# Optimization experiments

Hardware: AMD Instinct MI355X
Metric: run time of the kernel (lower is better)

Reference implementation:

```python
import jax, jax.numpy as jnp
import numpy as np

N = 50000      # nodes
E = 800000     # edges (avg degree 16)
DIN = 512      # input_dim
DH = 256       # hidden_dim
KMAX = 50      # max_clusters; K = max(5, min(50, ceil(N/50))) = 50 for N=50000


def _gcn_propagate(h, src, dst, n):
    """Symmetric-normalized GCN aggregation with self-loops (PyG GCNConv).
    h: already linearly transformed node features (n, d)."""
    loop = jnp.arange(n)
    s = jnp.concatenate([src, loop])
    d = jnp.concatenate([dst, loop])
    deg = jax.ops.segment_sum(jnp.ones_like(d, dtype=h.dtype), d, num_segments=n)
    dinv = jnp.where(deg > 0, deg ** -0.5, 0.0)
    norm = dinv[s] * dinv[d]                      # (E+N,)
    return jax.ops.segment_sum(norm[:, None] * h[s], d, num_segments=n)


def setup_inputs() -> dict:
    key = jax.random.key(0)
    ks = jax.random.split(key, 6)
    x = jax.random.normal(ks[0], (N, DIN), dtype=jnp.float32)
    edge_index = jax.random.randint(ks[1], (2, E), 0, N, dtype=jnp.int64)
    positions = jax.random.uniform(ks[2], (N, 2), dtype=jnp.float32)
    # GCNConv params (glorot-ish weights, zero bias as in PyG init)
    W1 = jax.random.normal(ks[3], (DIN, DH), dtype=jnp.float32) * np.float32(1.0 / np.sqrt(DIN))
    b1 = jnp.zeros((DH,), dtype=jnp.float32)
    W2 = jax.random.normal(ks[4], (DH, KMAX), dtype=jnp.float32) * np.float32(1.0 / np.sqrt(DH))
    b2 = jnp.zeros((KMAX,), dtype=jnp.float32)
    spatial_weight = jnp.asarray(1.0, dtype=jnp.float32)
    return {"x": x, "positions": positions, "W1": W1, "b1": b1,
            "W2": W2, "b2": b2, "spatial_weight": spatial_weight,
            "edge_index": edge_index}


def reference(x, positions, W1, b1, W2, b2, spatial_weight, edge_index):
    src, dst = edge_index[0], edge_index[1]
    n = x.shape[0]
    # layer 1: GCNConv(input_dim -> hidden_dim) + ReLU
    h = jax.nn.relu(_gcn_propagate(x @ W1, src, dst, n) + b1)
    # layer 2: GCNConv(hidden_dim -> max_clusters)
    s = _gcn_propagate(h @ W2, src, dst, n) + b2
    # K = max(5, min(50, ceil(N/50))) = 50 here -> s[:, :K] is identity slice
    S = jax.nn.softmax(s[:, :KMAX], axis=1)       # (N, K), Eq. 7
    # spatial loss (Eq. 9): softmax > 0 always, so the >0 guards are no-ops
    d2 = jnp.sum((positions[src] - positions[dst]) ** 2, axis=1)   # (E,) squared dist
    dot = jnp.sum(S[src] * S[dst], axis=1)                          # (E,) sum_k S_ik S_jk
    L_spatial = spatial_weight * jnp.sum(d2 * dot) / src.shape[0]
    return S, L_spatial
```

## Files before the change

### kernel.cpp

```cpp
#include <hip/hip_runtime.h>
#include <math.h>


typedef __attribute__((ext_vector_type(8))) short bf16x8;
typedef __attribute__((ext_vector_type(4))) float f32x4;
typedef __attribute__((ext_vector_type(4))) unsigned int u32x4;
typedef _Float16 f16;
typedef __attribute__((ext_vector_type(2))) _Float16 f16x2;
typedef __attribute__((ext_vector_type(4))) _Float16 f16x4;
typedef __attribute__((ext_vector_type(8))) _Float16 f16x8;

__device__ inline unsigned short f32_to_bf16(float f) {
    unsigned u = __float_as_uint(f);
    unsigned r = u + 0x7FFFu + ((u >> 16) & 1u);
    return (unsigned short)(r >> 16);
}
__device__ inline float bf16_to_f32(unsigned short h) {
    return __uint_as_float((unsigned)h << 16);
}

__device__ inline void glds16(const void* g, void* l) {
    __builtin_amdgcn_global_load_lds(
        (const __attribute__((address_space(1))) unsigned int*)g,
        (__attribute__((address_space(3))) unsigned int*)l, 16, 0, 0);
}

__global__ void detect_i64_kernel(const unsigned* __restrict__ w, int* __restrict__ flag) {
    __shared__ int red[256];
    int cnt = 0;
    for (int i = threadIdx.x; i < 4096; i += 256)
        cnt += (w[2 * i + 1] == 0u) ? 1 : 0;
    red[threadIdx.x] = cnt;
    __syncthreads();
    for (int s = 128; s > 0; s >>= 1) {
        if ((int)threadIdx.x < s) red[threadIdx.x] += red[threadIdx.x + s];
        __syncthreads();
    }
    if (threadIdx.x == 0) *flag = (red[0] > 2048) ? 1 : 0;
}

__global__ void convert_edges_kernel(const void* __restrict__ ei, int* __restrict__ es,
                                     int* __restrict__ ed, int* __restrict__ cnt,
                                     int E, const int* __restrict__ flag) {
    int idx = blockIdx.x * blockDim.x + threadIdx.x;
    if (idx >= 2 * E) return;
    int v;
    if (*flag) v = (int)((const long long*)ei)[idx];
    else       v = ((const int*)ei)[idx];
    if (idx < E) es[idx] = v;
    else { ed[idx - E] = v; atomicAdd(&cnt[v], 1); }
}

__global__ __launch_bounds__(1024) void scan_block_kernel(const int* __restrict__ cnt,
        int* __restrict__ row_ptr, int* __restrict__ btot, int n) {
    __shared__ int buf[1024];
    int i = blockIdx.x * 1024 + threadIdx.x;
    buf[threadIdx.x] = (i < n) ? cnt[i] : 0;
    __syncthreads();
    for (int off = 1; off < 1024; off <<= 1) {
        int t = ((int)threadIdx.x >= off) ? buf[threadIdx.x - off] : 0;
        __syncthreads();
        buf[threadIdx.x] += t;
        __syncthreads();
    }
    if (i < n) row_ptr[i + 1] = buf[threadIdx.x];
    if (threadIdx.x == 1023) btot[blockIdx.x] = buf[1023];
}

__global__ __launch_bounds__(1024) void scan_tops_kernel(int* __restrict__ btot, int nb) {
    __shared__ int buf[1024];
    buf[threadIdx.x] = ((int)threadIdx.x < nb) ? btot[threadIdx.x] : 0;
    __syncthreads();
    for (int off = 1; off < 1024; off <<= 1) {
        int t = ((int)threadIdx.x >= off) ? buf[threadIdx.x - off] : 0;
        __syncthreads();
        buf[threadIdx.x] += t;
        __syncthreads();
    }
    if ((int)threadIdx.x < nb) btot[threadIdx.x] = buf[threadIdx.x];
}

__global__ void scan_finalize_kernel(int* __restrict__ row_ptr, const int* __restrict__ btot,
        const int* __restrict__ cnt, int* __restrict__ cursor, float* __restrict__ dinv, int n) {
    int i = blockIdx.x * blockDim.x + threadIdx.x;
    if (i >= n) return;
    int blk = i >> 10;
    int off = blk ? btot[blk - 1] : 0;
    int incl = row_ptr[i + 1] + off;
    row_ptr[i + 1] = incl;
    cursor[i] = incl - cnt[i];
    dinv[i] = rsqrtf((float)(cnt[i] + 1));
    if (i == 0) row_ptr[0] = 0;
}

__global__ void scatter_kernel(const int* __restrict__ es, const int* __restrict__ ed,
                               const float* __restrict__ dinv, int* __restrict__ cursor,
                               int* __restrict__ csr_src, float* __restrict__ csr_nrm, int E) {
    int e = blockIdx.x * blockDim.x + threadIdx.x;
    if (e < E) {
        int s = es[e];
        int d = ed[e];
        int p = atomicAdd(&cursor[d], 1);
        csr_src[p] = s;
        csr_nrm[p] = dinv[s];
    }
}

__global__ void wsplit_kernel(const float* __restrict__ W,
                              unsigned short* __restrict__ Th,
                              unsigned short* __restrict__ Tl, int K, int N, int nk) {
    int idx = blockIdx.x * 256 + threadIdx.x;
    if (idx >= K * N) return;
    int k = idx / N, n = idx % N;
    float f = W[idx];
    unsigned short h = f32_to_bf16(f);
    unsigned short l = f32_to_bf16(f - bf16_to_f32(h));
    int p = n >> 7, np = n & 127, t = k >> 5, kg = (k & 31) >> 3, ke = k & 7;
    size_t o = ((size_t)((p * nk + t) * 4 + kg) << 10) + np * 8 + ke;
    Th[o] = h;
    Tl[o] = l;
}

__global__ void wsplit2_kernel(const float* __restrict__ W2,
                               f16* __restrict__ W2t_hi, f16* __restrict__ W2t_lo,
                               int K, int NC) {
    int idx = blockIdx.x * 256 + threadIdx.x;
    if (idx >= 64 * K) return;
    int n = idx / K, k = idx % K;
    float v = (n < NC) ? W2[(size_t)k * NC + n] : 0.f;
    f16 h = (f16)v;
    W2t_hi[idx] = h;
    W2t_lo[idx] = (f16)(v - (float)h);
}

#define G1_BM 128
#define G1_BN 128
#define G1_BK 32

__global__ __launch_bounds__(256) void gemm1_mfma(
        const float* __restrict__ X, const unsigned short* __restrict__ WtH,
        const unsigned short* __restrict__ WtL, f16* __restrict__ C,
        int M, int K, int N) {
    __shared__ __align__(16) unsigned char lds[32768];

    const int tid  = threadIdx.x;
    const int lane = tid & 63;
    const int wave = tid >> 6;
    const int wm   = wave & 1;
    const int wn   = wave >> 1;
    const int m0   = blockIdx.x * G1_BM;
    const int pn   = blockIdx.y;
    const int nk   = K / G1_BK;

    const float* Xbase[4];
    #pragma unroll
    for (int i = 0; i < 4; ++i) {
        int c   = i * 256 + tid;
        int row = c >> 3;
        int sl  = (c & 7) ^ (row & 7);
        int gr  = m0 + row;
        if (gr > M - 1) gr = M - 1;
        Xbase[i] = X + (size_t)gr * K + sl * 4;
    }
    const unsigned short* BhBase = WtH + ((size_t)pn * nk << 12) + (size_t)tid * 8;
    const unsigned short* BlBase = WtL + ((size_t)pn * nk << 12) + (size_t)tid * 8;

    f32x4 acc[4][4] = {};
    const int kq   = lane >> 4;
    const int frow = lane & 15;
    const int bOff = 16384 + (kq << 11) + ((wn * 64 + frow) << 4);

    for (int t = 0; t < nk; ++t) {
        const int k0 = t * G1_BK;
        #pragma unroll
        for (int i = 0; i < 4; ++i)
            glds16(Xbase[i] + k0, lds + i * 4096 + wave * 1024);
        const unsigned short* bh = BhBase + (size_t)t * 4096;
        const unsigned short* bl = BlBase + (size_t)t * 4096;
        glds16(bh,        lds + 16384 + wave * 1024);
        glds16(bh + 2048, lds + 20480 + wave * 1024);
        glds16(bl,        lds + 24576 + wave * 1024);
        glds16(bl + 2048, lds + 28672 + wave * 1024);
        __syncthreads();

        bf16x8 bhf[4], blf[4];
        #pragma unroll
        for (int nn = 0; nn < 4; ++nn) {
            bhf[nn] = *(const bf16x8*)(lds + bOff + nn * 256);
            blf[nn] = *(const bf16x8*)(lds + bOff + 8192 + nn * 256);
        }
        #pragma unroll
        for (int mm = 0; mm < 4; ++mm) {
            int ra = wm * 64 + mm * 16 + frow;
            int rb = ra << 7;
            int sw = (ra & 7) << 4;
            int s0 = kq << 1;
            f32x4 p0 = *(const f32x4*)(lds + rb + ((s0 << 4) ^ sw));
            f32x4 p1 = *(const f32x4*)(lds + rb + (((s0 + 1) << 4) ^ sw));
            float f[8] = {p0[0], p0[1], p0[2], p0[3], p1[0], p1[1], p1[2], p1[3]};
            u32x4 hv, lv;
            #pragma unroll
            for (int p = 0; p < 4; ++p) {
                unsigned b0 = __float_as_uint(f[2 * p]);
                unsigned b1 = __float_as_uint(f[2 * p + 1]);
                hv[p] = __builtin_amdgcn_perm(b1, b0, 0x07060302u);
                float l0 = f[2 * p]     - __uint_as_float(b0 & 0xFFFF0000u);
                float l1 = f[2 * p + 1] - __uint_as_float(b1 & 0xFFFF0000u);
                lv[p] = __builtin_amdgcn_perm(__float_as_uint(l1),
                                              __float_as_uint(l0), 0x07060302u);
            }
            union { u32x4 u; bf16x8 b; } ah, al;
            ah.u = hv; al.u = lv;
            #pragma unroll
            for (int nn = 0; nn < 4; ++nn)
                acc[mm][nn] = __builtin_amdgcn_mfma_f32_16x16x32_bf16(ah.b, bhf[nn], acc[mm][nn], 0, 0, 0);
            #pragma unroll
            for (int nn = 0; nn < 4; ++nn)
                acc[mm][nn] = __builtin_amdgcn_mfma_f32_16x16x32_bf16(ah.b, blf[nn], acc[mm][nn], 0, 0, 0);
            #pragma unroll
            for (int nn = 0; nn < 4; ++nn)
                acc[mm][nn] = __builtin_amdgcn_mfma_f32_16x16x32_bf16(al.b, bhf[nn], acc[mm][nn], 0, 0, 0);
        }
        __syncthreads();
    }

    const int n0 = pn * G1_BN;
    #pragma unroll
    for (int mm = 0; mm < 4; ++mm) {
        #pragma unroll
        for (int i = 0; i < 4; ++i) {
            int gr = m0 + wm * 64 + mm * 16 + kq * 4 + i;
            if (gr >= M) continue;
            #pragma unroll
            for (int nn = 0; nn < 4; ++nn) {
                int gc = n0 + wn * 64 + nn * 16 + frow;
                C[(size_t)gr * N + gc] = (f16)acc[mm][nn][i];
            }
        }
    }
}

__device__ inline float4 ld_h4(const f16x4* __restrict__ p) {
    f16x4 v = *p;
    return make_float4((float)v.x, (float)v.y, (float)v.z, (float)v.w);
}

__global__ __launch_bounds__(256) void agg1_gemm2_kernel(
        const f16* __restrict__ h0, const float* __restrict__ dinv,
        const int* __restrict__ row_ptr, const int* __restrict__ csr_src,
        const float* __restrict__ csr_nrm, const float* __restrict__ b1,
        const f16* __restrict__ W2t_hi, const f16* __restrict__ W2t_lo,
        f16* __restrict__ g, int n, int K, int KC) {
    __shared__ __align__(16) f16 hs[32][264];

    const int tid  = threadIdx.x;
    const int lane = tid & 63;
    const int wave = tid >> 6;
    const int base = blockIdx.x * 32;

    const f16x4* h0v = (const f16x4*)h0;
    float4 bb = ((const float4*)b1)[lane];
    for (int i = 0; i < 8; ++i) {
        int wid = base + wave * 8 + i;
        f16x4 out = {0, 0, 0, 0};
        if (wid < n) {
            float di = dinv[wid];
            float4 v = ld_h4(&h0v[(size_t)wid * 64 + lane]);
            float self = di * di;
            float4 acc;
            acc.x = self * v.x; acc.y = self * v.y; acc.z = self * v.z; acc.w = self * v.w;
            int beg = row_ptr[wid], end = row_ptr[wid + 1];
            int j = beg;
            for (; j + 4 <= end; j += 4) {
                int s0 = csr_src[j],     s1 = csr_src[j + 1];
                int s2 = csr_src[j + 2], s3 = csr_src[j + 3];
                float n0 = csr_nrm[j] * di,     n1 = csr_nrm[j + 1] * di;
                float n2 = csr_nrm[j + 2] * di, n3 = csr_nrm[j + 3] * di;
                float4 u0 = ld_h4(&h0v[(size_t)s0 * 64 + lane]);
                float4 u1 = ld_h4(&h0v[(size_t)s1 * 64 + lane]);
                float4 u2 = ld_h4(&h0v[(size_t)s2 * 64 + lane]);
                float4 u3 = ld_h4(&h0v[(size_t)s3 * 64 + lane]);
                acc.x = fmaf(n0, u0.x, acc.x); acc.y = fmaf(n0, u0.y, acc.y);
                acc.z = fmaf(n0, u0.z, acc.z); acc.w = fmaf(n0, u0.w, acc.w);
                acc.x = fmaf(n1, u1.x, acc.x); acc.y = fmaf(n1, u1.y, acc.y);
                acc.z = fmaf(n1, u1.z, acc.z); acc.w = fmaf(n1, u1.w, acc.w);
                acc.x = fmaf(n2, u2.x, acc.x); acc.y = fmaf(n2, u2.y, acc.y);
                acc.z = fmaf(n2, u2.z, acc.z); acc.w = fmaf(n2, u2.w, acc.w);
                acc.x = fmaf(n3, u3.x, acc.x); acc.y = fmaf(n3, u3.y, acc.y);
                acc.z = fmaf(n3, u3.z, acc.z); acc.w = fmaf(n3, u3.w, acc.w);
            }
            for (; j < end; ++j) {
                int s0 = csr_src[j];
                float n0 = csr_nrm[j] * di;
                float4 u0 = ld_h4(&h0v[(size_t)s0 * 64 + lane]);
                acc.x = fmaf(n0, u0.x, acc.x); acc.y = fmaf(n0, u0.y, acc.y);
                acc.z = fmaf(n0, u0.z, acc.z); acc.w = fmaf(n0, u0.w, acc.w);
            }
            out.x = (f16)fmaxf(acc.x + bb.x, 0.f);
            out.y = (f16)fmaxf(acc.y + bb.y, 0.f);
            out.z = (f16)fmaxf(acc.z + bb.z, 0.f);
            out.w = (f16)fmaxf(acc.w + bb.w, 0.f);
        }
        *(f16x4*)&hs[wave * 8 + i][lane * 4] = out;
    }
    __syncthreads();

    const int wm   = wave & 1;
    const int wn   = wave >> 1;
    const int kq   = lane >> 4;
    const int frow = lane & 15;
    const int koff = kq * 8;

    f32x4 acc2[2] = {};
    const f16* bh_base[2];
    const f16* bl_base[2];
    #pragma unroll
    for (int nn = 0; nn < 2; ++nn) {
        int r = wn * 32 + nn * 16 + frow;
        bh_base[nn] = W2t_hi + (size_t)r * K + koff;
        bl_base[nn] = W2t_lo + (size_t)r * K + koff;
    }

    for (int t = 0; t < K / 32; ++t) {
        const int kk = t * 32;
        f16x8 a = *(const f16x8*)&hs[wm * 16 + frow][kk + koff];
        #pragma unroll
        for (int nn = 0; nn < 2; ++nn) {
            f16x8 bh = *(const f16x8*)(bh_base[nn] + kk);
            f16x8 bl = *(const f16x8*)(bl_base[nn] + kk);
            acc2[nn] = __builtin_amdgcn_mfma_f32_16x16x32_f16(a, bh, acc2[nn], 0, 0, 0);
            acc2[nn] = __builtin_amdgcn_mfma_f32_16x16x32_f16(a, bl, acc2[nn], 0, 0, 0);
        }
    }

    #pragma unroll
    for (int i = 0; i < 4; ++i) {
        int gr = base + wm * 16 + kq * 4 + i;
        if (gr >= n) continue;
        #pragma unroll
        for (int nn = 0; nn < 2; ++nn) {
            int gc = wn * 32 + nn * 16 + frow;
            if (gc < KC) g[(size_t)gr * KC + gc] = (f16)acc2[nn][i];
        }
    }
}

__global__ __launch_bounds__(256) void agg2_softmax_kernel(const f16* __restrict__ g,
        const float* __restrict__ dinv, const int* __restrict__ row_ptr,
        const int* __restrict__ csr_src, const float* __restrict__ csr_nrm,
        const float* __restrict__ b2, float* __restrict__ S, f16* __restrict__ Sh,
        int n, int KC) {
    int wid = (int)((blockIdx.x * (size_t)blockDim.x + threadIdx.x) >> 6);
    int lane = threadIdx.x & 63;
    if (wid >= n) return;
    bool act = lane < KC;
    size_t gidx = act ? (size_t)lane : 0;
    float di = dinv[wid];
    float a0 = 0.f, a1 = 0.f, a2 = 0.f, a3 = 0.f;
    if (act) a0 = di * di * (float)g[(size_t)wid * KC + lane];
    int beg = row_ptr[wid], end = row_ptr[wid + 1];
    int j = beg;
    for (; j + 4 <= end; j += 4) {
        int s0 = csr_src[j], s1 = csr_src[j + 1], s2 = csr_src[j + 2], s3 = csr_src[j + 3];
        float n0 = csr_nrm[j]     * di;
        float n1 = csr_nrm[j + 1] * di;
        float n2 = csr_nrm[j + 2] * di;
        float n3 = csr_nrm[j + 3] * di;
        float g0 = (float)g[(size_t)s0 * KC + gidx];
        float g1 = (float)g[(size_t)s1 * KC + gidx];
        float g2 = (float)g[(size_t)s2 * KC + gidx];
        float g3 = (float)g[(size_t)s3 * KC + gidx];
        a0 = fmaf(n0, g0, a0);
        a1 = fmaf(n1, g1, a1);
        a2 = fmaf(n2, g2, a2);
        a3 = fmaf(n3, g3, a3);
    }
    for (; j < end; ++j) {
        int s0 = csr_src[j];
        float n0 = csr_nrm[j] * di;
        a0 = fmaf(n0, (float)g[(size_t)s0 * KC + gidx], a0);
    }
    float acc = (a0 + a1) + (a2 + a3);
    float val = act ? (acc + b2[lane]) : -INFINITY;
    float m = val;
    #pragma unroll
    for (int o = 32; o > 0; o >>= 1) m = fmaxf(m, __shfl_xor(m, o));
    float e = act ? expf(val - m) : 0.f;
    float ssum = e;
    #pragma unroll
    for (int o = 32; o > 0; o >>= 1) ssum += __shfl_xor(ssum, o);
    {
        float sv = act ? (e / ssum) : 0.f;
        if (act) S[(size_t)wid * KC + lane] = sv;
        Sh[(size_t)wid * 64 + lane] = (f16)sv;
    }
}

__global__ __launch_bounds__(256) void loss_partial_kernel(const int* __restrict__ es,
        const int* __restrict__ ed, const float* __restrict__ pos,
        const f16* __restrict__ Sh, float* __restrict__ parts, int E) {
    float local = 0.f;
    int stride = gridDim.x * blockDim.x;
    for (int e = blockIdx.x * blockDim.x + threadIdx.x; e < E; e += stride) {
        int s = es[e], d = ed[e];
        float2 ps = ((const float2*)pos)[s];
        float2 pd = ((const float2*)pos)[d];
        float dx = ps.x - pd.x, dy = ps.y - pd.y;
        float d2 = dx * dx + dy * dy;
        const f16x8* Sa = (const f16x8*)(Sh + (size_t)s * 64);
        const f16x8* Sb = (const f16x8*)(Sh + (size_t)d * 64);
        float dot = 0.f;
        #pragma unroll
        for (int q = 0; q < 7; ++q) {
            f16x8 a = Sa[q], b = Sb[q];
            #pragma unroll
            for (int k = 0; k < 8; ++k)
                dot = fmaf((float)a[k], (float)b[k], dot);
        }
        local = fmaf(d2, dot, local);
    }
    __shared__ float red[256];
    red[threadIdx.x] = local;
    __syncthreads();
    for (int s = 128; s > 0; s >>= 1) {
        if ((int)threadIdx.x < s) red[threadIdx.x] += red[threadIdx.x + s];
        __syncthreads();
    }
    if (threadIdx.x == 0) parts[blockIdx.x] = red[0];
}

__global__ __launch_bounds__(1024) void loss_final_kernel(const float* __restrict__ parts,
        const float* __restrict__ sw, float* __restrict__ out, float invE) {
    __shared__ float red[1024];
    red[threadIdx.x] = parts[threadIdx.x];
    __syncthreads();
    for (int s = 512; s > 0; s >>= 1) {
        if ((int)threadIdx.x < s) red[threadIdx.x] += red[threadIdx.x + s];
        __syncthreads();
    }
    if (threadIdx.x == 0) out[0] = sw[0] * red[0] * invE;
}

extern "C" void kernel_launch(void* const* d_in, const int* in_sizes, int n_in,
                              void* d_out, int out_size, void* d_ws, size_t ws_size,
                              hipStream_t stream) {
    const float* x   = (const float*)d_in[0];
    const float* pos = (const float*)d_in[1];
    const float* W1  = (const float*)d_in[2];
    const float* b1  = (const float*)d_in[3];
    const float* W2  = (const float*)d_in[4];
    const float* b2  = (const float*)d_in[5];
    const float* sw  = (const float*)d_in[6];
    const void*  ei  = d_in[7];

    const int DH  = in_sizes[3];
    const int KC  = in_sizes[5];
    const int DIN = in_sizes[2] / DH;
    const int n   = in_sizes[0] / DIN;
    const int E   = in_sizes[7] / 2;

    char* p = (char*)d_ws;
    auto alloc = [&](size_t bytes) {
        char* r = p;
        p += (bytes + 255) & ~(size_t)255;
        return r;
    };
    int*   flag    = (int*)alloc(256);
    int*   es      = (int*)alloc((size_t)E * 4);
    int*   ed      = (int*)alloc((size_t)E * 4);
    int*   cnt     = (int*)alloc((size_t)n * 4);
    int*   cursor  = (int*)alloc((size_t)n * 4);
    int*   row_ptr = (int*)alloc(((size_t)n + 1) * 4);
    int*   btot    = (int*)alloc(1024 * 4);
    int*   csr     = (int*)alloc((size_t)E * 4);
    float* csr_nrm = (float*)alloc((size_t)E * 4);
    float* dinv    = (float*)alloc((size_t)n * 4);
    float* parts   = (float*)alloc(1024 * 4);
    unsigned short* Wt_hi = (unsigned short*)alloc((size_t)DIN * DH * 2);
    unsigned short* Wt_lo = (unsigned short*)alloc((size_t)DIN * DH * 2);
    f16*   W2t_hi  = (f16*)alloc((size_t)64 * DH * 2);
    f16*   W2t_lo  = (f16*)alloc((size_t)64 * DH * 2);
    f16*   h0      = (f16*)alloc((size_t)n * DH * 2);
    f16*   g       = (f16*)alloc((size_t)n * KC * 2);
    f16*   Sh      = (f16*)alloc((size_t)n * 64 * 2);

    float* S    = (float*)d_out;
    float* Lout = S + (size_t)n * KC;

    const int nb = (n + 1023) / 1024;
    const int nk = DIN / G1_BK;

    hipMemsetAsync(cnt, 0, (size_t)n * 4, stream);
    detect_i64_kernel<<<1, 256, 0, stream>>>((const unsigned*)ei, flag);
    convert_edges_kernel<<<(2 * E + 255) / 256, 256, 0, stream>>>(ei, es, ed, cnt, E, flag);
    scan_block_kernel<<<nb, 1024, 0, stream>>>(cnt, row_ptr, btot, n);
    scan_tops_kernel<<<1, 1024, 0, stream>>>(btot, nb);
    scan_finalize_kernel<<<(n + 255) / 256, 256, 0, stream>>>(row_ptr, btot, cnt, cursor, dinv, n);
    scatter_kernel<<<(E + 255) / 256, 256, 0, stream>>>(es, ed, dinv, cursor, csr, csr_nrm, E);

    wsplit_kernel<<<(DIN * DH + 255) / 256, 256, 0, stream>>>(W1, Wt_hi, Wt_lo, DIN, DH, nk);
    wsplit2_kernel<<<(64 * DH + 255) / 256, 256, 0, stream>>>(W2, W2t_hi, W2t_lo, DH, KC);

    dim3 g1((n + G1_BM - 1) / G1_BM, DH / G1_BN);
    gemm1_mfma<<<g1, 256, 0, stream>>>(x, Wt_hi, Wt_lo, h0, n, DIN, DH);

    agg1_gemm2_kernel<<<(n + 31) / 32, 256, 0, stream>>>(
        h0, dinv, row_ptr, csr, csr_nrm, b1, W2t_hi, W2t_lo, g, n, DH, KC);

    agg2_softmax_kernel<<<(int)(((size_t)n * 64 + 255) / 256), 256, 0, stream>>>(
        g, dinv, row_ptr, csr, csr_nrm, b2, S, Sh, n, KC);

    loss_partial_kernel<<<1024, 256, 0, stream>>>(es, ed, pos, Sh, parts, E);
    loss_final_kernel<<<1, 1024, 0, stream>>>(parts, sw, Lout, 1.0f / (float)E);
}
```

Baseline: 330.1 us.

## Use 16-byte half-wave gathers in aggregation and wave-cooperative loss edge dots

The layer-1 aggregation now has each half-wave load whole 256-dim neighbour rows as f16x8 (16-byte) vectors, so one wave handles two edges at once and the halves are combined with a cross-half shuffle. The loss kernel switches from one thread per edge, each reading a full 128-byte row serially, to 32 lanes per edge reading coalesced f16x2 slices and reducing with shuffles. Both changes aim to make the random row gathers wider and coalesced. The cost is extra shuffle reductions and lanes that sit idle on odd-length neighbour tails.

```diff
diff --git a/kernel.cpp b/kernel.cpp
--- a/kernel.cpp
+++ b/kernel.cpp
@@ -240,11 +240,6 @@
     }
 }
 
-__device__ inline float4 ld_h4(const f16x4* __restrict__ p) {
-    f16x4 v = *p;
-    return make_float4((float)v.x, (float)v.y, (float)v.z, (float)v.w);
-}
-
 __global__ __launch_bounds__(256) void agg1_gemm2_kernel(
         const f16* __restrict__ h0, const float* __restrict__ dinv,
         const int* __restrict__ row_ptr, const int* __restrict__ csr_src,
@@ -257,51 +252,57 @@
     const int lane = tid & 63;
     const int wave = tid >> 6;
     const int base = blockIdx.x * 32;
-
-    const f16x4* h0v = (const f16x4*)h0;
-    float4 bb = ((const float4*)b1)[lane];
+    const int c    = lane & 31;
+    const int hf   = lane >> 5;
+
+    const f16x8* h0v8 = (const f16x8*)h0;
+
+    float4 bA = ((const float4*)b1)[c * 2];
+    float4 bB = ((const float4*)b1)[c * 2 + 1];
+    float bb[8] = {bA.x, bA.y, bA.z, bA.w, bB.x, bB.y, bB.z, bB.w};
+
     for (int i = 0; i < 8; ++i) {
         int wid = base + wave * 8 + i;
-        f16x4 out = {0, 0, 0, 0};
+        float acc[8] = {};
         if (wid < n) {
             float di = dinv[wid];
-            float4 v = ld_h4(&h0v[(size_t)wid * 64 + lane]);
-            float self = di * di;
-            float4 acc;
-            acc.x = self * v.x; acc.y = self * v.y; acc.z = self * v.z; acc.w = self * v.w;
+            f16x8 vs = h0v8[(size_t)wid * 32 + c];
+            float selfm = (hf == 0) ? di * di : 0.f;
+            #pragma unroll
+            for (int q = 0; q < 8; ++q) acc[q] = selfm * (float)vs[q];
             int beg = row_ptr[wid], end = row_ptr[wid + 1];
             int j = beg;
             for (; j + 4 <= end; j += 4) {
-                int s0 = csr_src[j],     s1 = csr_src[j + 1];
-                int s2 = csr_src[j + 2], s3 = csr_src[j + 3];
-                float n0 = csr_nrm[j] * di,     n1 = csr_nrm[j + 1] * di;
-                float n2 = csr_nrm[j + 2] * di, n3 = csr_nrm[j + 3] * di;
-                float4 u0 = ld_h4(&h0v[(size_t)s0 * 64 + lane]);
-                float4 u1 = ld_h4(&h0v[(size_t)s1 * 64 + lane]);
-                float4 u2 = ld_h4(&h0v[(size_t)s2 * 64 + lane]);
-                float4 u3 = ld_h4(&h0v[(size_t)s3 * 64 + lane]);
-                acc.x = fmaf(n0, u0.x, acc.x); acc.y = fmaf(n0, u0.y, acc.y);
-                acc.z = fmaf(n0, u0.z, acc.z); acc.w = fmaf(n0, u0.w, acc.w);
-                acc.x = fmaf(n1, u1.x, acc.x); acc.y = fmaf(n1, u1.y, acc.y);
-                acc.z = fmaf(n1, u1.z, acc.z); acc.w = fmaf(n1, u1.w, acc.w);
-                acc.x = fmaf(n2, u2.x, acc.x); acc.y = fmaf(n2, u2.y, acc.y);
-                acc.z = fmaf(n2, u2.z, acc.z); acc.w = fmaf(n2, u2.w, acc.w);
-                acc.x = fmaf(n3, u3.x, acc.x); acc.y = fmaf(n3, u3.y, acc.y);
-                acc.z = fmaf(n3, u3.z, acc.z); acc.w = fmaf(n3, u3.w, acc.w);
+                int   sA = csr_src[j + hf];
+                int   sB = csr_src[j + 2 + hf];
+                float nA = csr_nrm[j + hf] * di;
+                float nB = csr_nrm[j + 2 + hf] * di;
+                f16x8 uA = h0v8[(size_t)sA * 32 + c];
+                f16x8 uB = h0v8[(size_t)sB * 32 + c];
+                #pragma unroll
+                for (int q = 0; q < 8; ++q) acc[q] = fmaf(nA, (float)uA[q], acc[q]);
+                #pragma unroll
+                for (int q = 0; q < 8; ++q) acc[q] = fmaf(nB, (float)uB[q], acc[q]);
             }
-            for (; j < end; ++j) {
-                int s0 = csr_src[j];
-                float n0 = csr_nrm[j] * di;
-                float4 u0 = ld_h4(&h0v[(size_t)s0 * 64 + lane]);
-                acc.x = fmaf(n0, u0.x, acc.x); acc.y = fmaf(n0, u0.y, acc.y);
-                acc.z = fmaf(n0, u0.z, acc.z); acc.w = fmaf(n0, u0.w, acc.w);
+            for (; j < end; j += 2) {
+                int  jj = j + hf;
+                bool vld = jj < end;
+                int   sA = csr_src[vld ? jj : j];
+                float nA = vld ? csr_nrm[jj] * di : 0.f;
+                f16x8 uA = h0v8[(size_t)sA * 32 + c];
+                #pragma unroll
+                for (int q = 0; q < 8; ++q) acc[q] = fmaf(nA, (float)uA[q], acc[q]);
             }
-            out.x = (f16)fmaxf(acc.x + bb.x, 0.f);
-            out.y = (f16)fmaxf(acc.y + bb.y, 0.f);
-            out.z = (f16)fmaxf(acc.z + bb.z, 0.f);
-            out.w = (f16)fmaxf(acc.w + bb.w, 0.f);
-        }
-        *(f16x4*)&hs[wave * 8 + i][lane * 4] = out;
+        }
+        #pragma unroll
+        for (int q = 0; q < 8; ++q) acc[q] += __shfl_xor(acc[q], 32);
+        if (hf == 0) {
+            f16x8 o;
+            #pragma unroll
+            for (int q = 0; q < 8; ++q)
+                o[q] = (wid < n) ? (f16)fmaxf(acc[q] + bb[q], 0.f) : (f16)0.f;
+            *(f16x8*)&hs[wave * 8 + i][c * 8] = o;
+        }
     }
     __syncthreads();
 
@@ -399,25 +400,29 @@
 __global__ __launch_bounds__(256) void loss_partial_kernel(const int* __restrict__ es,
         const int* __restrict__ ed, const float* __restrict__ pos,
         const f16* __restrict__ Sh, float* __restrict__ parts, int E) {
+    const int lane = threadIdx.x & 63;
+    const int grp  = lane >> 5;
+    const int c    = lane & 31;
+    const int gw   = (int)((blockIdx.x * (size_t)blockDim.x + threadIdx.x) >> 6);
+    const int nw   = (int)(gridDim.x * (blockDim.x >> 6));
+
     float local = 0.f;
-    int stride = gridDim.x * blockDim.x;
-    for (int e = blockIdx.x * blockDim.x + threadIdx.x; e < E; e += stride) {
-        int s = es[e], d = ed[e];
-        float2 ps = ((const float2*)pos)[s];
-        float2 pd = ((const float2*)pos)[d];
-        float dx = ps.x - pd.x, dy = ps.y - pd.y;
-        float d2 = dx * dx + dy * dy;
-        const f16x8* Sa = (const f16x8*)(Sh + (size_t)s * 64);
-        const f16x8* Sb = (const f16x8*)(Sh + (size_t)d * 64);
-        float dot = 0.f;
-        #pragma unroll
-        for (int q = 0; q < 7; ++q) {
-            f16x8 a = Sa[q], b = Sb[q];
-            #pragma unroll
-            for (int k = 0; k < 8; ++k)
-                dot = fmaf((float)a[k], (float)b[k], dot);
-        }
-        local = fmaf(d2, dot, local);
+    for (int base = gw * 2; base < E; base += nw * 2) {
+        int e = base + grp;
+        bool v = e < E;
+        int s = 0, d = 0;
+        if (v) { s = es[e]; d = ed[e]; }
+        f16x2 a = *(const f16x2*)(Sh + (size_t)s * 64 + c * 2);
+        f16x2 b = *(const f16x2*)(Sh + (size_t)d * 64 + c * 2);
+        float p = fmaf((float)a.x, (float)b.x, (float)a.y * (float)b.y);
+        #pragma unroll
+        for (int o = 16; o > 0; o >>= 1) p += __shfl_xor(p, o);
+        if (v && c == 0) {
+            float2 ps = ((const float2*)pos)[s];
+            float2 pd = ((const float2*)pos)[d];
+            float dx = ps.x - pd.x, dy = ps.y - pd.y;
+            local = fmaf(dx * dx + dy * dy, p, local);
+        }
     }
     __shared__ float red[256];
     red[threadIdx.x] = local;
```

Result: slower. 397.0 us (+20.3%).
